# Performance work log

Hardware: AMD Instinct MI355X
Metric: run time of the kernel (lower is better)

The kernel has to match this reference:

```python
import jax, jax.numpy as jnp
from jax import lax
import numpy as np

N_ATOMS = 8192
N_FREE = 4096
ATOM_MASS = 1.0


def setup_inputs() -> dict:
    key = jax.random.key(0)
    k1, k2, k3 = jax.random.split(key, 3)
    q = jax.random.normal(k1, (N_FREE, 3), dtype=jnp.float32)
    qd = jax.random.normal(k2, (N_FREE, 3), dtype=jnp.float32)
    x0 = jax.random.normal(k3, (N_ATOMS, 3), dtype=jnp.float32)
    free_idx = jnp.arange(N_FREE, dtype=jnp.int64 if jax.config.jax_enable_x64 else jnp.int32)
    return {"q": q, "qd": qd, "x0": x0, "free_idx": free_idx}


def reference(q, qd, x0, free_idx):
    # x = x0 with free rows replaced by q; constrained atoms have zero velocity,
    # so T = m/2 * sum(qd^2) exactly (xd is zero elsewhere).
    x = x0.at[free_idx].set(q)
    T = ATOM_MASS / 2 * jnp.sum(qd ** 2)

    # All-pairs potential sum_{i<j} 1/r_ij, then module returns 2*V,
    # i.e. the full sum over ordered pairs i != j of 1/r_ij.
    # Vectorized via ||xi - xj||^2 = |xi|^2 + |xj|^2 - 2 xi.xj (single [N,N] matmul).
    x2 = jnp.sum(x * x, axis=1)                      # [N]
    r2 = x2[:, None] + x2[None, :] - 2.0 * (x @ x.T)  # [N, N]
    n = x.shape[0]
    diag = jnp.eye(n, dtype=bool)
    r2_safe = jnp.where(diag, 1.0, jnp.maximum(r2, 1e-12))
    rinv = jnp.where(diag, 0.0, lax.rsqrt(r2_safe))   # 1/r_ij, zero on diagonal
    V2 = jnp.sum(rinv)                                # == 2 * sum_{i<j} 1/r_ij
    return T - V2
```

## Files before the change

kernel.cpp:

```cpp
#include <hip/hip_runtime.h>

#define NATOMS 8192
#define NFREE  4096

constexpr int TPB = 256;
constexpr int IPT = 4;
constexpr int TI  = TPB * IPT;
constexpr int JT  = 32;
constexpr int GI  = NATOMS / TI;
constexpr int GJ  = NATOMS / JT;
constexpr int TPS = TI / JT;
__device__ __constant__ const int S_START[GI + 1] = {0, 256, 480, 672, 832, 960, 1056, 1120, 1152};
constexpr int NVBLK = 1152;

typedef __attribute__((ext_vector_type(2))) float f32x2;

__device__ __forceinline__ f32x2 pk_fma_blo(f32x2 a, f32x2 b, f32x2 c) {
    f32x2 d;
    asm("v_pk_fma_f32 %0, %1, %2, %3 op_sel:[0,0,0] op_sel_hi:[1,0,1]"
        : "=v"(d) : "v"(a), "v"(b), "v"(c));
    return d;
}
__device__ __forceinline__ f32x2 pk_fma_bhi(f32x2 a, f32x2 b, f32x2 c) {
    f32x2 d;
    asm("v_pk_fma_f32 %0, %1, %2, %3 op_sel:[0,1,0] op_sel_hi:[1,1,1]"
        : "=v"(d) : "v"(a), "v"(b), "v"(c));
    return d;
}
__device__ __forceinline__ f32x2 pk_add_bhi(f32x2 a, f32x2 b) {
    f32x2 d;
    asm("v_pk_add_f32 %0, %1, %2 op_sel:[0,1] op_sel_hi:[1,1]"
        : "=v"(d) : "v"(a), "v"(b));
    return d;
}

__device__ __forceinline__ float wave_reduce(float v) {
#pragma unroll
    for (int off = 32; off > 0; off >>= 1)
        v += __shfl_down(v, off, 64);
    return v;
}

__global__ __launch_bounds__(TPB) void pair_kernel(const float* __restrict__ q,
                                                   const float* __restrict__ x0,
                                                   float* __restrict__ vpart) {
    __shared__ float4 sj[JT];
    const int bid = blockIdx.x;

    int x = 0;
#pragma unroll
    for (int e = 1; e < GI; ++e) x += (bid >= S_START[e]);
    const int y  = bid - S_START[x] + TPS * x;
    const int i0 = x * TI;
    const int j0 = y * JT;
    const int t  = threadIdx.x;

    if (t < JT) {
        const int ja = j0 + t;
        const float* p = (ja < NFREE) ? (q + 3 * ja) : (x0 + 3 * ja);
        float xx = p[0], yy = p[1], zz = p[2];
        sj[t] = make_float4(xx, yy, zz, fmaf(xx, xx, fmaf(yy, yy, zz * zz)));
    }

    const float* isrc = (i0 < NFREE) ? q : x0;
    f32x2 ax2[IPT / 2], ay2[IPT / 2], az2[IPT / 2], s2[IPT / 2];
    float acc[IPT];
    int m[IPT];
    const int rel0 = j0 - i0;
#pragma unroll
    for (int k = 0; k < IPT; ++k) {
        const int ia = i0 + t + k * TPB;
        float xx = isrc[3 * ia + 0], yy = isrc[3 * ia + 1], zz = isrc[3 * ia + 2];
        ax2[k / 2][k & 1] = -2.f * xx;
        ay2[k / 2][k & 1] = -2.f * yy;
        az2[k / 2][k & 1] = -2.f * zz;
        s2[k / 2][k & 1]  = fmaf(xx, xx, fmaf(yy, yy, zz * zz));
        acc[k] = 0.f;
        m[k] = t + k * TPB - rel0;
    }
    __syncthreads();

    if (rel0 < TI) {
#pragma unroll 8
        for (int j = 0; j < JT; ++j) {
            const float4 pj = sj[j];
            f32x2 pxy; pxy.x = pj.x; pxy.y = pj.y;
            f32x2 pzw; pzw.x = pj.z; pzw.y = pj.w;
#pragma unroll
            for (int g = 0; g < IPT / 2; ++g) {
                f32x2 d = pk_fma_blo(ax2[g], pxy, s2[g]);
                d = pk_fma_bhi(ay2[g], pxy, d);
                d = pk_fma_blo(az2[g], pzw, d);
                d = pk_add_bhi(d, pzw);
                float r0 = __builtin_amdgcn_rsqf(d.x);
                float r1 = __builtin_amdgcn_rsqf(d.y);
                acc[2 * g + 0] += (m[2 * g + 0] < j) ? r0 : 0.f;
                acc[2 * g + 1] += (m[2 * g + 1] < j) ? r1 : 0.f;
            }
        }
    } else {
#pragma unroll 8
        for (int j = 0; j < JT; ++j) {
            const float4 pj = sj[j];
            f32x2 pxy; pxy.x = pj.x; pxy.y = pj.y;
            f32x2 pzw; pzw.x = pj.z; pzw.y = pj.w;
#pragma unroll
            for (int g = 0; g < IPT / 2; ++g) {
                f32x2 d = pk_fma_blo(ax2[g], pxy, s2[g]);
                d = pk_fma_bhi(ay2[g], pxy, d);
                d = pk_fma_blo(az2[g], pzw, d);
                d = pk_add_bhi(d, pzw);
                acc[2 * g + 0] += __builtin_amdgcn_rsqf(d.x);
                acc[2 * g + 1] += __builtin_amdgcn_rsqf(d.y);
            }
        }
    }

    float v = (acc[0] + acc[1]) + (acc[2] + acc[3]);
    v = wave_reduce(v);
    __shared__ float s[TPB / 64];
    int lane = t & 63, wid = t >> 6;
    if (lane == 0) s[wid] = v;
    __syncthreads();
    if (t == 0)
        vpart[bid] = (s[0] + s[1]) + (s[2] + s[3]);
}

__global__ void finalize(const float* __restrict__ vpart,
                         const float4* __restrict__ qd4,
                         float* __restrict__ out) {
    float v = 0.f;
    for (int i = threadIdx.x; i < NVBLK; i += TPB) v += vpart[i];
    float tq = 0.f;
    for (int i = threadIdx.x; i < (NFREE * 3) / 4; i += TPB) {
        float4 u = qd4[i];
        tq += fmaf(u.x, u.x, fmaf(u.y, u.y, fmaf(u.z, u.z, u.w * u.w)));
    }
    v = wave_reduce(v);
    tq = wave_reduce(tq);
    __shared__ float sv[TPB / 64], st[TPB / 64];
    int lane = threadIdx.x & 63, wid = threadIdx.x >> 6;
    if (lane == 0) { sv[wid] = v; st[wid] = tq; }
    __syncthreads();
    if (threadIdx.x == 0) {
        float V = (sv[0] + sv[1]) + (sv[2] + sv[3]);
        float T = (st[0] + st[1]) + (st[2] + st[3]);
        out[0] = 0.5f * T - 2.0f * V;
    }
}

extern "C" void kernel_launch(void* const* d_in, const int* in_sizes, int n_in,
                              void* d_out, int out_size, void* d_ws, size_t ws_size,
                              hipStream_t stream) {
    const float* q  = (const float*)d_in[0];
    const float* qd = (const float*)d_in[1];
    const float* x0 = (const float*)d_in[2];
    float* out = (float*)d_out;

    float* vpart = (float*)d_ws;

    pair_kernel<<<NVBLK, TPB, 0, stream>>>(q, x0, vpart);
    finalize<<<1, TPB, 0, stream>>>(vpart, (const float4*)qd, out);
}
```

Baseline: 17.30 us.

## Fuse finalize into pair kernel with atomic slots and last-block reduction

Drops the separate finalize launch. Each block atomically adds its partial sum into one of 8 slots and bumps a counter, and the last block to finish computes the kinetic term and writes the output. A memset of the slots and counter now runs before the kernel, and the change also fully unrolls the j loop and sets the launch bound to 5 blocks. It trades one kernel launch for a memset plus atomics, and the float atomics make the summation order nondeterministic.

```diff
diff --git a/kernel.cpp b/kernel.cpp
--- a/kernel.cpp
+++ b/kernel.cpp
@@ -12,6 +12,7 @@
 constexpr int TPS = TI / JT;
 __device__ __constant__ const int S_START[GI + 1] = {0, 256, 480, 672, 832, 960, 1056, 1120, 1152};
 constexpr int NVBLK = 1152;
+constexpr int NSLOT = 8;
 
 typedef __attribute__((ext_vector_type(2))) float f32x2;
 
@@ -41,9 +42,12 @@
     return v;
 }
 
-__global__ __launch_bounds__(TPB) void pair_kernel(const float* __restrict__ q,
-                                                   const float* __restrict__ x0,
-                                                   float* __restrict__ vpart) {
+__global__ __launch_bounds__(TPB, 5) void pair_kernel(const float* __restrict__ q,
+                                                      const float* __restrict__ x0,
+                                                      const float4* __restrict__ qd4,
+                                                      float* __restrict__ vslot,
+                                                      int* __restrict__ counter,
+                                                      float* __restrict__ out) {
     __shared__ float4 sj[JT];
     const int bid = blockIdx.x;
 
@@ -81,7 +85,7 @@
     __syncthreads();
 
     if (rel0 < TI) {
-#pragma unroll 8
+#pragma unroll
         for (int j = 0; j < JT; ++j) {
             const float4 pj = sj[j];
             f32x2 pxy; pxy.x = pj.x; pxy.y = pj.y;
@@ -99,7 +103,7 @@
             }
         }
     } else {
-#pragma unroll 8
+#pragma unroll
         for (int j = 0; j < JT; ++j) {
             const float4 pj = sj[j];
             f32x2 pxy; pxy.x = pj.x; pxy.y = pj.y;
@@ -119,33 +123,36 @@
     float v = (acc[0] + acc[1]) + (acc[2] + acc[3]);
     v = wave_reduce(v);
     __shared__ float s[TPB / 64];
+    __shared__ bool sdone;
     int lane = t & 63, wid = t >> 6;
     if (lane == 0) s[wid] = v;
     __syncthreads();
-    if (t == 0)
-        vpart[bid] = (s[0] + s[1]) + (s[2] + s[3]);
-}
+    if (t == 0) {
+        float vtot = (s[0] + s[1]) + (s[2] + s[3]);
+        atomicAdd(&vslot[bid & (NSLOT - 1)], vtot);
+        asm volatile("s_waitcnt vmcnt(0)" ::: "memory");
+        int old = atomicAdd(counter, 1);
+        sdone = (old == NVBLK - 1);
+    }
+    __syncthreads();
 
-__global__ void finalize(const float* __restrict__ vpart,
-                         const float4* __restrict__ qd4,
-                         float* __restrict__ out) {
-    float v = 0.f;
-    for (int i = threadIdx.x; i < NVBLK; i += TPB) v += vpart[i];
-    float tq = 0.f;
-    for (int i = threadIdx.x; i < (NFREE * 3) / 4; i += TPB) {
-        float4 u = qd4[i];
-        tq += fmaf(u.x, u.x, fmaf(u.y, u.y, fmaf(u.z, u.z, u.w * u.w)));
-    }
-    v = wave_reduce(v);
-    tq = wave_reduce(tq);
-    __shared__ float sv[TPB / 64], st[TPB / 64];
-    int lane = threadIdx.x & 63, wid = threadIdx.x >> 6;
-    if (lane == 0) { sv[wid] = v; st[wid] = tq; }
-    __syncthreads();
-    if (threadIdx.x == 0) {
-        float V = (sv[0] + sv[1]) + (sv[2] + sv[3]);
-        float T = (st[0] + st[1]) + (st[2] + st[3]);
-        out[0] = 0.5f * T - 2.0f * V;
+    if (sdone) {
+        float tq = 0.f;
+        for (int i = t; i < (NFREE * 3) / 4; i += TPB) {
+            float4 u = qd4[i];
+            tq += fmaf(u.x, u.x, fmaf(u.y, u.y, fmaf(u.z, u.z, u.w * u.w)));
+        }
+        tq = wave_reduce(tq);
+        if (lane == 0) s[wid] = tq;
+        __syncthreads();
+        if (t == 0) {
+            float T = (s[0] + s[1]) + (s[2] + s[3]);
+            float V = 0.f;
+#pragma unroll
+            for (int i = 0; i < NSLOT; ++i)
+                V += __hip_atomic_load(&vslot[i], __ATOMIC_RELAXED, __HIP_MEMORY_SCOPE_AGENT);
+            out[0] = 0.5f * T - 2.0f * V;
+        }
     }
 }
 
@@ -157,8 +164,9 @@
     const float* x0 = (const float*)d_in[2];
     float* out = (float*)d_out;
 
-    float* vpart = (float*)d_ws;
+    float* vslot   = (float*)d_ws;
+    int*   counter = (int*)d_ws + NSLOT;
 
-    pair_kernel<<<NVBLK, TPB, 0, stream>>>(q, x0, vpart);
-    finalize<<<1, TPB, 0, stream>>>(vpart, (const float4*)qd, out);
+    hipMemsetAsync(d_ws, 0, (NSLOT + 1) * sizeof(float), stream);
+    pair_kernel<<<NVBLK, TPB, 0, stream>>>(q, x0, (const float4*)qd, vslot, counter, out);
 }
```

After: 44.72 us. +158.5%, slower.
